# Performance work log

Hardware: AMD Instinct MI355X
Metric: run time of the kernel (lower is better)

The kernel has to match this reference:

```python
import jax, jax.numpy as jnp
import numpy as np

N, NFEAT, NHID, NCLASS, H1 = 4096, 512, 64, 16, 8
GAIN = 1.414  # xavier gain used by the torch module
NEG_SLOPE = 0.2
MASK_VAL = -1e10


def _xavier(k, shape):
    fan_in, fan_out = shape[-2], shape[-1]
    lim = GAIN * (6.0 / (fan_in + fan_out)) ** 0.5
    return jax.random.uniform(k, shape, jnp.float32, -lim, lim)


def setup_inputs() -> dict:
    key = jax.random.key(0)
    ks = jax.random.split(key, 10)
    return {
        "x": jax.random.normal(ks[0], (N, NFEAT), jnp.float32),
        "adj": jax.random.randint(ks[1], (N, N), 0, 2, jnp.int32),
        # layer-1 parameters, stacked over H1 heads
        "W1": _xavier(ks[2], (H1, NFEAT, NHID)),
        "b1": jnp.zeros((H1, NHID), jnp.float32),
        "as1": _xavier(ks[3], (H1, NHID, 1))[..., 0],
        "an1": _xavier(ks[4], (H1, NHID, 1))[..., 0],
        # layer-2 parameters (single head, input = H1*NHID due to concat)
        "W2": _xavier(ks[5], (H1 * NHID, NCLASS)),
        "b2": jnp.zeros((NCLASS,), jnp.float32),
        "as2": _xavier(ks[6], (NCLASS, 1))[:, 0],
        "an2": _xavier(ks[7], (NCLASS, 1))[:, 0],
    }


def gat_layer(X, adj_pos, W, b, a_s, a_n):
    # X: [N, Fin], W: [Fin, Fout], a_s/a_n: [Fout], adj_pos: [N, N] bool
    feats = X @ W                                        # [N, Fout]
    s = feats @ a_s                                      # [N]
    nb = feats @ a_n                                     # [N]
    attn = jax.nn.leaky_relu(s[:, None] + nb[None, :], NEG_SLOPE)  # [N, N]
    attn = jnp.where(adj_pos, attn, MASK_VAL)
    attn = jax.nn.softmax(attn, axis=-1)
    # dropout on attn/feats is a no-op in eval mode
    return attn @ feats + b                              # [N, Fout]


def reference(x, adj, W1, b1, as1, an1, W2, b2, as2, an2):
    adj_pos = adj > 0
    # x dropout is a no-op in eval mode
    layer1 = jax.vmap(gat_layer, in_axes=(None, None, 0, 0, 0, 0))
    h = jax.nn.relu(layer1(x, adj_pos, W1, b1, as1, an1))    # [H1, N, NHID]
    h = jnp.transpose(h, (1, 0, 2)).reshape(N, H1 * NHID)    # concat heads on dim 1
    h = jax.nn.elu(h)
    out = jax.nn.relu(gat_layer(h, adj_pos, W2, b2, as2, an2))  # [N, NCLASS]
    return jax.nn.log_softmax(out, axis=1)
```

## Files before the change

### kernel.cpp

```cpp
#include <hip/hip_runtime.h>

#define NN 4096
#define NFEAT 512
#define NHID 64
#define H1 8
#define NCLS 16
#define BND 40.0f

typedef short bf16x8 __attribute__((ext_vector_type(8)));
typedef float f32x4 __attribute__((ext_vector_type(4)));

__device__ __forceinline__ unsigned short f2bf(float f) {
    unsigned u = __float_as_uint(f);
    u += 0x7fffu + ((u >> 16) & 1u);
    return (unsigned short)(u >> 16);
}
__device__ __forceinline__ float leaky(float v) { return fmaxf(v, 0.2f * v); }
__device__ __forceinline__ unsigned pkbf(float lo, float hi) {
    return __builtin_amdgcn_perm(__float_as_uint(hi) + 0x8000u,
                                 __float_as_uint(lo) + 0x8000u, 0x07060302u);
}
__device__ __forceinline__ bf16x8 mk8(unsigned a, unsigned b, unsigned c, unsigned d) {
    union { unsigned u[4]; bf16x8 v; } cv;
    cv.u[0] = a; cv.u[1] = b; cv.u[2] = c; cv.u[3] = d; return cv.v;
}
__device__ __forceinline__ unsigned bmask(unsigned b, int i) {
#if __has_builtin(__builtin_amdgcn_sbfe)
    return (unsigned)__builtin_amdgcn_sbfe((int)b, (unsigned)i, 1u);
#else
    return 0u - ((b >> i) & 1u);
#endif
}

__global__ __launch_bounds__(256)
void k_prep(const int* __restrict__ adj, unsigned long long* __restrict__ bits,
            const float* __restrict__ W1, unsigned short* __restrict__ w1f)
{
    __shared__ float wt[64][65];
    const int t = threadIdx.x, bx = blockIdx.x;
    if (bx < NN) {
        const int wv = t >> 6, lane = t & 63;
        const int* ap = adj + (size_t)bx * NN;
        for (int w = wv; w < 64; w += 4) {
            unsigned long long m = __ballot(ap[w * 64 + lane] > 0);
            if (lane == 0) bits[(size_t)bx * 64 + w] = m;
        }
        return;
    }
    const int kt = (bx - NN) & 7, h = (bx - NN) >> 3;
    #pragma unroll
    for (int i = 0; i < 4; ++i) {
        const int f = t + 256 * i;
        const int r = f >> 4, c4 = f & 15;
        const float4 v = *(const float4*)(W1 + ((size_t)(h * NFEAT) + kt * 64 + r) * NHID + c4 * 4);
        wt[r][c4 * 4 + 0] = v.x; wt[r][c4 * 4 + 1] = v.y;
        wt[r][c4 * 4 + 2] = v.z; wt[r][c4 * 4 + 3] = v.w;
    }
    __syncthreads();
    #pragma unroll
    for (int s = 0; s < 2; ++s) {
        const int o = t + s * 256;
        const int kg2 = o >> 8, rem = o & 255;
        const int nt = rem >> 6, lane2 = rem & 63;
        const int qq = lane2 >> 4, nn = lane2 & 15;
        const int kl = kg2 * 32 + qq * 8;
        const int c = nt * 16 + nn;
        uint4 w;
        w.x = pkbf(wt[kl + 0][c], wt[kl + 1][c]);
        w.y = pkbf(wt[kl + 2][c], wt[kl + 3][c]);
        w.z = pkbf(wt[kl + 4][c], wt[kl + 5][c]);
        w.w = pkbf(wt[kl + 6][c], wt[kl + 7][c]);
        *(uint4*)(w1f + (((size_t)h * 16 + kt * 2 + kg2) * 4 + nt) * 512 + lane2 * 8) = w;
    }
}

__global__ __launch_bounds__(256)
void k_feats1(const float* __restrict__ x, const unsigned short* __restrict__ w1f,
              const float* __restrict__ as1, const float* __restrict__ an1,
              unsigned short* __restrict__ f1t, float* __restrict__ s1,
              float* __restrict__ F1a, float* __restrict__ F2a)
{
    const int t = threadIdx.x, wv = t >> 6, lane = t & 63;
    const int q = lane >> 4, n = lane & 15;
    const int h = blockIdx.y, R0 = blockIdx.x * 64;
    const int row = R0 + wv * 16 + n;
    const float* ap = x + (size_t)row * NFEAT;
    const unsigned short* wp = w1f + (size_t)h * 16 * 4 * 512 + lane * 8;
    f32x4 acc[4] = {{0.f,0.f,0.f,0.f},{0.f,0.f,0.f,0.f},{0.f,0.f,0.f,0.f},{0.f,0.f,0.f,0.f}};
    #pragma unroll 4
    for (int kg = 0; kg < 16; ++kg) {
        const float4 xa = *(const float4*)(ap + kg * 32 + q * 8);
        const float4 xb = *(const float4*)(ap + kg * 32 + q * 8 + 4);
        const bf16x8 af = mk8(pkbf(xa.x, xa.y), pkbf(xa.z, xa.w),
                              pkbf(xb.x, xb.y), pkbf(xb.z, xb.w));
        #pragma unroll
        for (int nt = 0; nt < 4; ++nt) {
            const bf16x8 bf = *(const bf16x8*)(wp + (size_t)(kg * 4 + nt) * 512);
            acc[nt] = __builtin_amdgcn_mfma_f32_16x16x32_bf16(af, bf, acc[nt], 0, 0, 0);
        }
    }
    {
        const int jg = R0 + wv * 16 + q * 4;
        const int jt = jg >> 5, jo = jg & 31;
        #pragma unroll
        for (int nt = 0; nt < 4; ++nt) {
            uint2 w;
            w.x = pkbf(acc[nt][0], acc[nt][1]);
            w.y = pkbf(acc[nt][2], acc[nt][3]);
            *(uint2*)(f1t + (((size_t)h * 128 + jt) * 64 + nt * 16 + n) * 32 + jo) = w;
        }
    }
    float asv[4], anv[4];
    #pragma unroll
    for (int nt = 0; nt < 4; ++nt) {
        asv[nt] = as1[h * NHID + nt * 16 + n];
        anv[nt] = an1[h * NHID + nt * 16 + n];
    }
    #pragma unroll
    for (int i = 0; i < 4; ++i) {
        float ps = acc[0][i]*asv[0] + acc[1][i]*asv[1] + acc[2][i]*asv[2] + acc[3][i]*asv[3];
        float pn = acc[0][i]*anv[0] + acc[1][i]*anv[1] + acc[2][i]*anv[2] + acc[3][i]*anv[3];
        #pragma unroll
        for (int off = 8; off > 0; off >>= 1) {
            ps += __shfl_xor(ps, off, 64);
            pn += __shfl_xor(pn, off, 64);
        }
        if (n == 0) {
            const int idx = R0 + wv * 16 + q * 4 + i;
            s1[h * NN + idx] = ps;
            F1a[h * NN + idx] = __expf(pn - BND);
            F2a[h * NN + idx] = __expf(0.2f * (pn - BND));
        }
    }
}

__global__ __launch_bounds__(512, 4)
void k_gat1(const unsigned short* __restrict__ f1t, const float* __restrict__ s1,
            const float* __restrict__ F1, const float* __restrict__ F2,
            const unsigned long long* __restrict__ abits, const float* __restrict__ b1,
            unsigned short* __restrict__ hcatb)
{
    __shared__ __align__(16) char smem[35328];
    float* fLds = (float*)smem;

    const int t = threadIdx.x, wv = t >> 6, lane = t & 63;
    const int q = lane >> 4, n = lane & 15;
    const int bid = blockIdx.x;
    const int h = bid & 7, R0 = (bid >> 3) * 32;
    const int rowA = R0 + n, rowB = R0 + 16 + n;

    const float vA = s1[h * NN + rowA] + BND, mhA = leaky(vA);
    const float vB = s1[h * NN + rowB] + BND, mhB = leaky(vB);
    const float E1A = __expf(vA - mhA), E2A = __expf(0.2f * vA - mhA);
    const float E1B = __expf(vB - mhB), E2B = __expf(0.2f * vB - mhB);

    const unsigned* arowA32 = (const unsigned*)abits + (size_t)rowA * 128 + wv * 16;
    const unsigned* arowB32 = (const unsigned*)abits + (size_t)rowB * 128 + wv * 16;
    const float* F1p = F1 + (size_t)h * NN + wv * 512;
    const float* F2p = F2 + (size_t)h * NN + wv * 512;

    float* myF = fLds + wv * 1024;
    {
        #pragma unroll
        for (int r = 0; r < 2; ++r) {
            *(float4*)(myF + r * 256 + lane * 4)       = *(const float4*)(F1p + r * 256 + lane * 4);
            *(float4*)(myF + 512 + r * 256 + lane * 4) = *(const float4*)(F2p + r * 256 + lane * 4);
        }
    }

    const unsigned short* vbase = f1t + ((size_t)h * 128 + wv * 16) * 2048 + n * 32 + q * 8;

    f32x4 accA[4] = {{0.f,0.f,0.f,0.f},{0.f,0.f,0.f,0.f},{0.f,0.f,0.f,0.f},{0.f,0.f,0.f,0.f}};
    f32x4 accB[4] = {{0.f,0.f,0.f,0.f},{0.f,0.f,0.f,0.f},{0.f,0.f,0.f,0.f},{0.f,0.f,0.f,0.f}};
    float lsA = 0.f, lsB = 0.f;

    bf16x8 vb[4];
    #pragma unroll
    for (int nt = 0; nt < 4; ++nt) vb[nt] = *(const bf16x8*)(vbase + nt * 512);
    unsigned aA = arowA32[0], aB = arowB32[0];

    #pragma unroll 2
    for (int it = 0; it < 16; ++it) {
        bf16x8 nb[4];
        unsigned aAn, aBn;
        if (it < 15) {
            const unsigned short* p = vbase + (size_t)(it + 1) * 2048;
            #pragma unroll
            for (int nt = 0; nt < 4; ++nt) nb[nt] = *(const bf16x8*)(p + nt * 512);
            aAn = arowA32[it + 1]; aBn = arowB32[it + 1];
        }
        const int j0 = it * 32, kb = q * 8;
        const float4 f1a = *(const float4*)(myF + j0 + kb);
        const float4 f1b = *(const float4*)(myF + j0 + kb + 4);
        const float4 f2a = *(const float4*)(myF + 512 + j0 + kb);
        const float4 f2b = *(const float4*)(myF + 512 + j0 + kb + 4);
        const float F1v[8] = {f1a.x, f1a.y, f1a.z, f1a.w, f1b.x, f1b.y, f1b.z, f1b.w};
        const float F2v[8] = {f2a.x, f2a.y, f2a.z, f2a.w, f2b.x, f2b.y, f2b.z, f2b.w};
        const unsigned bA8 = (aA >> kb) & 0xffu;
        const unsigned bB8 = (aB >> kb) & 0xffu;
        unsigned uA[4], uB[4];
        #pragma unroll
        for (int jp = 0; jp < 4; ++jp) {
            float a0 = fmaxf(E1A * F1v[2*jp],   E2A * F2v[2*jp]);
            float a1 = fmaxf(E1A * F1v[2*jp+1], E2A * F2v[2*jp+1]);
            a0 = __uint_as_float(__float_as_uint(a0) & bmask(bA8, 2*jp));
            a1 = __uint_as_float(__float_as_uint(a1) & bmask(bA8, 2*jp+1));
            lsA += a0 + a1;
            uA[jp] = pkbf(a0, a1);
            float b0  = fmaxf(E1B * F1v[2*jp],   E2B * F2v[2*jp]);
            float b1v = fmaxf(E1B * F1v[2*jp+1], E2B * F2v[2*jp+1]);
            b0  = __uint_as_float(__float_as_uint(b0)  & bmask(bB8, 2*jp));
            b1v = __uint_as_float(__float_as_uint(b1v) & bmask(bB8, 2*jp+1));
            lsB += b0 + b1v;
            uB[jp] = pkbf(b0, b1v);
        }
        const bf16x8 afA = mk8(uA[0], uA[1], uA[2], uA[3]);
        const bf16x8 afB = mk8(uB[0], uB[1], uB[2], uB[3]);
        #pragma unroll
        for (int nt = 0; nt < 4; ++nt) {
            accA[nt] = __builtin_amdgcn_mfma_f32_16x16x32_bf16(afA, vb[nt], accA[nt], 0, 0, 0);
            accB[nt] = __builtin_amdgcn_mfma_f32_16x16x32_bf16(afB, vb[nt], accB[nt], 0, 0, 0);
        }
        #pragma unroll
        for (int nt = 0; nt < 4; ++nt) vb[nt] = nb[nt];
        aA = aAn; aB = aBn;
    }

    lsA += __shfl_xor(lsA, 16, 64); lsA += __shfl_xor(lsA, 32, 64);
    lsB += __shfl_xor(lsB, 16, 64); lsB += __shfl_xor(lsB, 32, 64);

    __syncthreads();

    float (*cmbf)[16][68] = (float (*)[16][68])smem;
    float (*lwf)[16] = (float (*)[16])(smem + 8 * 16 * 68 * 4);

    #pragma unroll
    for (int nt = 0; nt < 4; ++nt)
        #pragma unroll
        for (int i = 0; i < 4; ++i)
            cmbf[wv][q * 4 + i][nt * 16 + n] = accA[nt][i];
    if (q == 0) lwf[wv][n] = lsA;
    __syncthreads();
    {
        const int r = t >> 5, c0 = (t & 31) * 2;
        float t0 = 0.f, t1 = 0.f, lt = 0.f;
        #pragma unroll
        for (int jj = 0; jj < 8; ++jj) {
            const float2 v = *(const float2*)&cmbf[jj][r][c0];
            t0 += v.x; t1 += v.y;
            lt += lwf[jj][r];
        }
        const float o0 = fmaxf(t0 / lt + b1[h * NHID + c0], 0.f);
        const float o1 = fmaxf(t1 / lt + b1[h * NHID + c0 + 1], 0.f);
        *(unsigned*)(hcatb + (size_t)(R0 + r) * (H1 * NHID) + h * NHID + c0) = pkbf(o0, o1);
    }
    __syncthreads();

    #pragma unroll
    for (int nt = 0; nt < 4; ++nt)
        #pragma unroll
        for (int i = 0; i < 4; ++i)
            cmbf[wv][q * 4 + i][nt * 16 + n] = accB[nt][i];
    if (q == 0) lwf[wv][n] = lsB;
    __syncthreads();
    {
        const int r = t >> 5, c0 = (t & 31) * 2;
        float t0 = 0.f, t1 = 0.f, lt = 0.f;
        #pragma unroll
        for (int jj = 0; jj < 8; ++jj) {
            const float2 v = *(const float2*)&cmbf[jj][r][c0];
            t0 += v.x; t1 += v.y;
            lt += lwf[jj][r];
        }
        const float o0 = fmaxf(t0 / lt + b1[h * NHID + c0], 0.f);
        const float o1 = fmaxf(t1 / lt + b1[h * NHID + c0 + 1], 0.f);
        *(unsigned*)(hcatb + (size_t)(R0 + 16 + r) * (H1 * NHID) + h * NHID + c0) = pkbf(o0, o1);
    }
}

__global__ __launch_bounds__(128)
void k_feats2(const unsigned short* __restrict__ hcatb, const float* __restrict__ W2,
              const float* __restrict__ as2, const float* __restrict__ an2,
              unsigned short* __restrict__ f2t, float* __restrict__ s2,
              float* __restrict__ F1b, float* __restrict__ F2b)
{
    __shared__ __align__(16) unsigned short w2T[NCLS][520];
    const int t = threadIdx.x, wv = t >> 6, lane = t & 63;
    const int q = lane >> 4, n = lane & 15;
    #pragma unroll
    for (int i = 0; i < 16; ++i) {
        const int f4 = t + 128 * i;
        const float4 v = ((const float4*)W2)[f4];
        const int k = f4 >> 2, c0 = (f4 & 3) * 4;
        w2T[c0 + 0][k] = f2bf(v.x); w2T[c0 + 1][k] = f2bf(v.y);
        w2T[c0 + 2][k] = f2bf(v.z); w2T[c0 + 3][k] = f2bf(v.w);
    }
    __syncthreads();

    const int R0 = blockIdx.x * 32;
    const int row = R0 + wv * 16 + n;
    const unsigned short* ap = hcatb + (size_t)row * NFEAT;
    f32x4 acc = {0.f, 0.f, 0.f, 0.f};
    #pragma unroll 4
    for (int k0 = 0; k0 < NFEAT; k0 += 32) {
        const bf16x8 af = *(const bf16x8*)(ap + k0 + q * 8);
        const bf16x8 bf = *(const bf16x8*)&w2T[n][k0 + q * 8];
        acc = __builtin_amdgcn_mfma_f32_16x16x32_bf16(af, bf, acc, 0, 0, 0);
    }
    uint2 w;
    w.x = pkbf(acc[0], acc[1]);
    w.y = pkbf(acc[2], acc[3]);
    *(uint2*)(f2t + ((size_t)blockIdx.x * 16 + n) * 32 + wv * 16 + q * 4) = w;
    const float asv = as2[n], anv = an2[n];
    #pragma unroll
    for (int i = 0; i < 4; ++i) {
        float ps = acc[i] * asv, pn = acc[i] * anv;
        #pragma unroll
        for (int off = 8; off > 0; off >>= 1) {
            ps += __shfl_xor(ps, off, 64);
            pn += __shfl_xor(pn, off, 64);
        }
        if (n == 0) {
            const int idx = R0 + wv * 16 + q * 4 + i;
            s2[idx] = ps;
            F1b[idx] = __expf(pn - BND);
            F2b[idx] = __expf(0.2f * (pn - BND));
        }
    }
}

__global__ __launch_bounds__(1024)
void k_gat2(const unsigned short* __restrict__ f2t, const float* __restrict__ s2,
            const float* __restrict__ F1, const float* __restrict__ F2,
            const unsigned long long* __restrict__ abits, const float* __restrict__ b2,
            float* __restrict__ out)
{
    __shared__ float cmb[16][16][17];
    __shared__ float lw[16][16];
    const int t = threadIdx.x, wv = t >> 6, lane = t & 63;
    const int q = lane >> 4, n = lane & 15;
    const int R0 = blockIdx.x * 16, row = R0 + n;
    const float v = s2[row] + BND, mhat = leaky(v);
    const float E1 = __expf(v - mhat), E2 = __expf(0.2f * v - mhat);
    const unsigned long long* arow = abits + (size_t)row * 64;

    f32x4 acc = {0.f, 0.f, 0.f, 0.f};
    float lsum = 0.f;
    const int jbeg = wv * 256;
    for (int j0 = jbeg; j0 < jbeg + 256; j0 += 64) {
        const unsigned long long a64 = arow[j0 >> 6];
        #pragma unroll
        for (int ch = 0; ch < 2; ++ch) {
            const int kb = ch * 32 + q * 8;
            const float4 f1a = *(const float4*)(F1 + j0 + kb);
            const float4 f1b = *(const float4*)(F1 + j0 + kb + 4);
            const float4 f2a = *(const float4*)(F2 + j0 + kb);
            const float4 f2b = *(const float4*)(F2 + j0 + kb + 4);
            const float F1v[8] = {f1a.x, f1a.y, f1a.z, f1a.w, f1b.x, f1b.y, f1b.z, f1b.w};
            const float F2v[8] = {f2a.x, f2a.y, f2a.z, f2a.w, f2b.x, f2b.y, f2b.z, f2b.w};
            const unsigned b8 = (unsigned)(a64 >> kb) & 0xffu;
            unsigned au[4];
            #pragma unroll
            for (int jp = 0; jp < 4; ++jp) {
                float p0 = fmaxf(E1 * F1v[2*jp],   E2 * F2v[2*jp]);
                float p1 = fmaxf(E1 * F1v[2*jp+1], E2 * F2v[2*jp+1]);
                p0 = __uint_as_float(__float_as_uint(p0) & bmask(b8, 2*jp));
                p1 = __uint_as_float(__float_as_uint(p1) & bmask(b8, 2*jp+1));
                lsum += p0 + p1;
                au[jp] = pkbf(p0, p1);
            }
            const bf16x8 af = mk8(au[0], au[1], au[2], au[3]);
            const bf16x8 bf = *(const bf16x8*)(f2t + ((size_t)((j0 >> 5) + ch) * 16 + n) * 32 + q * 8);
            acc = __builtin_amdgcn_mfma_f32_16x16x32_bf16(af, bf, acc, 0, 0, 0);
        }
    }
    lsum += __shfl_xor(lsum, 16, 64);
    lsum += __shfl_xor(lsum, 32, 64);
    #pragma unroll
    for (int i = 0; i < 4; ++i) cmb[wv][q * 4 + i][n] = acc[i];
    if (q == 0) lw[wv][n] = lsum;
    __syncthreads();

    if (t < 256) {
        const int r = t >> 4, c = t & 15;
        float tot = 0.f, lt = 0.f;
        #pragma unroll
        for (int w16 = 0; w16 < 16; ++w16) { tot += cmb[w16][r][c]; lt += lw[w16][r]; }
        float val = fmaxf(tot / lt + b2[c], 0.f);
        float mx = val;
        #pragma unroll
        for (int off = 1; off < 16; off <<= 1) mx = fmaxf(mx, __shfl_xor(mx, off, 64));
        const float e = __expf(val - mx);
        float se = e;
        #pragma unroll
        for (int off = 1; off < 16; off <<= 1) se += __shfl_xor(se, off, 64);
        out[(size_t)(R0 + r) * NCLS + c] = val - mx - __logf(se);
    }
}

extern "C" void kernel_launch(void* const* d_in, const int* in_sizes, int n_in,
                              void* d_out, int out_size, void* d_ws, size_t ws_size,
                              hipStream_t stream)
{
    const float* x   = (const float*)d_in[0];
    const int*   adj = (const int*)  d_in[1];
    const float* W1  = (const float*)d_in[2];
    const float* b1  = (const float*)d_in[3];
    const float* as1 = (const float*)d_in[4];
    const float* an1 = (const float*)d_in[5];
    const float* W2  = (const float*)d_in[6];
    const float* b2  = (const float*)d_in[7];
    const float* as2 = (const float*)d_in[8];
    const float* an2 = (const float*)d_in[9];
    float* out = (float*)d_out;

    char* ws = (char*)d_ws;
    unsigned long long* abits = (unsigned long long*)(ws);
    unsigned short* f1t   = (unsigned short*)(ws + (2u << 20));
    unsigned short* hcatb = (unsigned short*)(ws + (6u << 20));
    unsigned short* w1f   = (unsigned short*)(ws + (10u << 20));
    char* ws2 = ws + (10u << 20) + (512u << 10);
    float* s1   = (float*)(ws2);
    float* F1a  = (float*)(ws2 + (128u << 10));
    float* F2a  = (float*)(ws2 + (256u << 10));
    unsigned short* f2t = (unsigned short*)(ws2 + (384u << 10));
    float* s2   = (float*)(ws2 + (512u << 10));
    float* F1b  = (float*)(ws2 + (528u << 10));
    float* F2b  = (float*)(ws2 + (544u << 10));

    k_prep  <<<dim3(NN + 64),     256, 0, stream>>>(adj, abits, W1, w1f);
    k_feats1<<<dim3(NN / 64, H1), 256, 0, stream>>>(x, w1f, as1, an1, f1t, s1, F1a, F2a);
    k_gat1  <<<dim3(NN / 32 * H1), 512, 0, stream>>>(f1t, s1, F1a, F2a, abits, b1, hcatb);
    k_feats2<<<dim3(NN / 32),     128, 0, stream>>>(hcatb, W2, as2, an2, f2t, s2, F1b, F2b);
    k_gat2  <<<dim3(NN / 16),     1024, 0, stream>>>(f2t, s2, F1b, F2b, abits, b2, out);
}
```

Measured before the change: 213.0 us.

## Compute softmax row sums via MFMA with ones column and pack FP32 multiplies

Replaces the per-lane scalar accumulation of attention weights with an extra MFMA against a ones vector (only column 0 is nonzero), so the row-sum denominator comes out of the matrix unit. The exp-weight multiplies are rewritten as 2-wide float vectors so the compiler can use packed FP32 math. In the layer-1 kernel it also drops the register double-buffered prefetch of V fragments and loads them directly each iteration, which lowers register pressure but exposes load latency. The sum now uses bf16-rounded weights rather than fp32 values, so the denominator matches the numerator's precision.

```diff
diff --git a/kernel.cpp b/kernel.cpp
--- a/kernel.cpp
+++ b/kernel.cpp
@@ -9,6 +9,7 @@
 
 typedef short bf16x8 __attribute__((ext_vector_type(8)));
 typedef float f32x4 __attribute__((ext_vector_type(4)));
+typedef float f32x2 __attribute__((ext_vector_type(2)));
 
 __device__ __forceinline__ unsigned short f2bf(float f) {
     unsigned u = __float_as_uint(f);
@@ -151,8 +152,10 @@
 
     const float vA = s1[h * NN + rowA] + BND, mhA = leaky(vA);
     const float vB = s1[h * NN + rowB] + BND, mhB = leaky(vB);
-    const float E1A = __expf(vA - mhA), E2A = __expf(0.2f * vA - mhA);
-    const float E1B = __expf(vB - mhB), E2B = __expf(0.2f * vB - mhB);
+    const f32x2 e1a = {__expf(vA - mhA), __expf(vA - mhA)};
+    const f32x2 e2a = {__expf(0.2f * vA - mhA), __expf(0.2f * vA - mhA)};
+    const f32x2 e1b = {__expf(vB - mhB), __expf(vB - mhB)};
+    const f32x2 e2b = {__expf(0.2f * vB - mhB), __expf(0.2f * vB - mhB)};
 
     const unsigned* arowA32 = (const unsigned*)abits + (size_t)rowA * 128 + wv * 16;
     const unsigned* arowB32 = (const unsigned*)abits + (size_t)rowB * 128 + wv * 16;
@@ -170,64 +173,58 @@
 
     const unsigned short* vbase = f1t + ((size_t)h * 128 + wv * 16) * 2048 + n * 32 + q * 8;
 
+    const bf16x8 onesB = (n == 0) ? mk8(0x3f803f80u, 0x3f803f80u, 0x3f803f80u, 0x3f803f80u)
+                                  : mk8(0u, 0u, 0u, 0u);
+
     f32x4 accA[4] = {{0.f,0.f,0.f,0.f},{0.f,0.f,0.f,0.f},{0.f,0.f,0.f,0.f},{0.f,0.f,0.f,0.f}};
     f32x4 accB[4] = {{0.f,0.f,0.f,0.f},{0.f,0.f,0.f,0.f},{0.f,0.f,0.f,0.f},{0.f,0.f,0.f,0.f}};
-    float lsA = 0.f, lsB = 0.f;
-
-    bf16x8 vb[4];
-    #pragma unroll
-    for (int nt = 0; nt < 4; ++nt) vb[nt] = *(const bf16x8*)(vbase + nt * 512);
+    f32x4 accSA = {0.f,0.f,0.f,0.f}, accSB = {0.f,0.f,0.f,0.f};
+
     unsigned aA = arowA32[0], aB = arowB32[0];
 
     #pragma unroll 2
     for (int it = 0; it < 16; ++it) {
-        bf16x8 nb[4];
         unsigned aAn, aBn;
-        if (it < 15) {
-            const unsigned short* p = vbase + (size_t)(it + 1) * 2048;
-            #pragma unroll
-            for (int nt = 0; nt < 4; ++nt) nb[nt] = *(const bf16x8*)(p + nt * 512);
-            aAn = arowA32[it + 1]; aBn = arowB32[it + 1];
-        }
+        if (it < 15) { aAn = arowA32[it + 1]; aBn = arowB32[it + 1]; }
         const int j0 = it * 32, kb = q * 8;
         const float4 f1a = *(const float4*)(myF + j0 + kb);
         const float4 f1b = *(const float4*)(myF + j0 + kb + 4);
         const float4 f2a = *(const float4*)(myF + 512 + j0 + kb);
         const float4 f2b = *(const float4*)(myF + 512 + j0 + kb + 4);
-        const float F1v[8] = {f1a.x, f1a.y, f1a.z, f1a.w, f1b.x, f1b.y, f1b.z, f1b.w};
-        const float F2v[8] = {f2a.x, f2a.y, f2a.z, f2a.w, f2b.x, f2b.y, f2b.z, f2b.w};
+        f32x2 F1q[4], F2q[4];
+        F1q[0] = f32x2{f1a.x, f1a.y}; F1q[1] = f32x2{f1a.z, f1a.w};
+        F1q[2] = f32x2{f1b.x, f1b.y}; F1q[3] = f32x2{f1b.z, f1b.w};
+        F2q[0] = f32x2{f2a.x, f2a.y}; F2q[1] = f32x2{f2a.z, f2a.w};
+        F2q[2] = f32x2{f2b.x, f2b.y}; F2q[3] = f32x2{f2b.z, f2b.w};
         const unsigned bA8 = (aA >> kb) & 0xffu;
         const unsigned bB8 = (aB >> kb) & 0xffu;
         unsigned uA[4], uB[4];
         #pragma unroll
         for (int jp = 0; jp < 4; ++jp) {
-            float a0 = fmaxf(E1A * F1v[2*jp],   E2A * F2v[2*jp]);
-            float a1 = fmaxf(E1A * F1v[2*jp+1], E2A * F2v[2*jp+1]);
+            const f32x2 x1 = e1a * F1q[jp], x2 = e2a * F2q[jp];
+            float a0 = fmaxf(x1.x, x2.x), a1 = fmaxf(x1.y, x2.y);
             a0 = __uint_as_float(__float_as_uint(a0) & bmask(bA8, 2*jp));
             a1 = __uint_as_float(__float_as_uint(a1) & bmask(bA8, 2*jp+1));
-            lsA += a0 + a1;
             uA[jp] = pkbf(a0, a1);
-            float b0  = fmaxf(E1B * F1v[2*jp],   E2B * F2v[2*jp]);
-            float b1v = fmaxf(E1B * F1v[2*jp+1], E2B * F2v[2*jp+1]);
+            const f32x2 y1 = e1b * F1q[jp], y2 = e2b * F2q[jp];
+            float b0 = fmaxf(y1.x, y2.x), b1v = fmaxf(y1.y, y2.y);
             b0  = __uint_as_float(__float_as_uint(b0)  & bmask(bB8, 2*jp));
             b1v = __uint_as_float(__float_as_uint(b1v) & bmask(bB8, 2*jp+1));
-            lsB += b0 + b1v;
             uB[jp] = pkbf(b0, b1v);
         }
         const bf16x8 afA = mk8(uA[0], uA[1], uA[2], uA[3]);
         const bf16x8 afB = mk8(uB[0], uB[1], uB[2], uB[3]);
+        const unsigned short* bp = vbase + (size_t)it * 2048;
         #pragma unroll
         for (int nt = 0; nt < 4; ++nt) {
-            accA[nt] = __builtin_amdgcn_mfma_f32_16x16x32_bf16(afA, vb[nt], accA[nt], 0, 0, 0);
-            accB[nt] = __builtin_amdgcn_mfma_f32_16x16x32_bf16(afB, vb[nt], accB[nt], 0, 0, 0);
-        }
-        #pragma unroll
-        for (int nt = 0; nt < 4; ++nt) vb[nt] = nb[nt];
+            const bf16x8 bf = *(const bf16x8*)(bp + nt * 512);
+            accA[nt] = __builtin_amdgcn_mfma_f32_16x16x32_bf16(afA, bf, accA[nt], 0, 0, 0);
+            accB[nt] = __builtin_amdgcn_mfma_f32_16x16x32_bf16(afB, bf, accB[nt], 0, 0, 0);
+        }
+        accSA = __builtin_amdgcn_mfma_f32_16x16x32_bf16(afA, onesB, accSA, 0, 0, 0);
+        accSB = __builtin_amdgcn_mfma_f32_16x16x32_bf16(afB, onesB, accSB, 0, 0, 0);
         aA = aAn; aB = aBn;
     }
-
-    lsA += __shfl_xor(lsA, 16, 64); lsA += __shfl_xor(lsA, 32, 64);
-    lsB += __shfl_xor(lsB, 16, 64); lsB += __shfl_xor(lsB, 32, 64);
 
     __syncthreads();
 
@@ -239,7 +236,10 @@
         #pragma unroll
         for (int i = 0; i < 4; ++i)
             cmbf[wv][q * 4 + i][nt * 16 + n] = accA[nt][i];
-    if (q == 0) lwf[wv][n] = lsA;
+    if (n == 0) {
+        #pragma unroll
+        for (int i = 0; i < 4; ++i) lwf[wv][q * 4 + i] = accSA[i];
+    }
     __syncthreads();
     {
         const int r = t >> 5, c0 = (t & 31) * 2;
@@ -261,7 +261,10 @@
         #pragma unroll
         for (int i = 0; i < 4; ++i)
             cmbf[wv][q * 4 + i][nt * 16 + n] = accB[nt][i];
-    if (q == 0) lwf[wv][n] = lsB;
+    if (n == 0) {
+        #pragma unroll
+        for (int i = 0; i < 4; ++i) lwf[wv][q * 4 + i] = accSB[i];
+    }
     __syncthreads();
     {
         const int r = t >> 5, c0 = (t & 31) * 2;
@@ -341,11 +344,15 @@
     const int q = lane >> 4, n = lane & 15;
     const int R0 = blockIdx.x * 16, row = R0 + n;
     const float v = s2[row] + BND, mhat = leaky(v);
-    const float E1 = __expf(v - mhat), E2 = __expf(0.2f * v - mhat);
+    const f32x2 e1 = {__expf(v - mhat), __expf(v - mhat)};
+    const f32x2 e2 = {__expf(0.2f * v - mhat), __expf(0.2f * v - mhat)};
     const unsigned long long* arow = abits + (size_t)row * 64;
 
+    const bf16x8 onesB = (n == 0) ? mk8(0x3f803f80u, 0x3f803f80u, 0x3f803f80u, 0x3f803f80u)
+                                  : mk8(0u, 0u, 0u, 0u);
+
     f32x4 acc = {0.f, 0.f, 0.f, 0.f};
-    float lsum = 0.f;
+    f32x4 accS = {0.f, 0.f, 0.f, 0.f};
     const int jbeg = wv * 256;
     for (int j0 = jbeg; j0 < jbeg + 256; j0 += 64) {
         const unsigned long long a64 = arow[j0 >> 6];
@@ -356,29 +363,33 @@
             const float4 f1b = *(const float4*)(F1 + j0 + kb + 4);
             const float4 f2a = *(const float4*)(F2 + j0 + kb);
             const float4 f2b = *(const float4*)(F2 + j0 + kb + 4);
-            const float F1v[8] = {f1a.x, f1a.y, f1a.z, f1a.w, f1b.x, f1b.y, f1b.z, f1b.w};
-            const float F2v[8] = {f2a.x, f2a.y, f2a.z, f2a.w, f2b.x, f2b.y, f2b.z, f2b.w};
+            f32x2 F1q[4], F2q[4];
+            F1q[0] = f32x2{f1a.x, f1a.y}; F1q[1] = f32x2{f1a.z, f1a.w};
+            F1q[2] = f32x2{f1b.x, f1b.y}; F1q[3] = f32x2{f1b.z, f1b.w};
+            F2q[0] = f32x2{f2a.x, f2a.y}; F2q[1] = f32x2{f2a.z, f2a.w};
+            F2q[2] = f32x2{f2b.x, f2b.y}; F2q[3] = f32x2{f2b.z, f2b.w};
             const unsigned b8 = (unsigned)(a64 >> kb) & 0xffu;
             unsigned au[4];
             #pragma unroll
             for (int jp = 0; jp < 4; ++jp) {
-                float p0 = fmaxf(E1 * F1v[2*jp],   E2 * F2v[2*jp]);
-                float p1 = fmaxf(E1 * F1v[2*jp+1], E2 * F2v[2*jp+1]);
+                const f32x2 x1 = e1 * F1q[jp], x2 = e2 * F2q[jp];
+                float p0 = fmaxf(x1.x, x2.x), p1 = fmaxf(x1.y, x2.y);
                 p0 = __uint_as_float(__float_as_uint(p0) & bmask(b8, 2*jp));
                 p1 = __uint_as_float(__float_as_uint(p1) & bmask(b8, 2*jp+1));
-                lsum += p0 + p1;
                 au[jp] = pkbf(p0, p1);
             }
             const bf16x8 af = mk8(au[0], au[1], au[2], au[3]);
             const bf16x8 bf = *(const bf16x8*)(f2t + ((size_t)((j0 >> 5) + ch) * 16 + n) * 32 + q * 8);
             acc = __builtin_amdgcn_mfma_f32_16x16x32_bf16(af, bf, acc, 0, 0, 0);
-        }
-    }
-    lsum += __shfl_xor(lsum, 16, 64);
-    lsum += __shfl_xor(lsum, 32, 64);
+            accS = __builtin_amdgcn_mfma_f32_16x16x32_bf16(af, onesB, accS, 0, 0, 0);
+        }
+    }
     #pragma unroll
     for (int i = 0; i < 4; ++i) cmb[wv][q * 4 + i][n] = acc[i];
-    if (q == 0) lw[wv][n] = lsum;
+    if (n == 0) {
+        #pragma unroll
+        for (int i = 0; i < 4; ++i) lw[wv][q * 4 + i] = accS[i];
+    }
     __syncthreads();
 
     if (t < 256) {
```

Measured after the change: 214.3 us. No clear change (+0.6%).
